# Kernel tuning notes

Hardware: AMD Instinct MI355X
Metric: run time of the kernel (lower is better)

The kernel has to match this reference:

```python
import jax, jax.numpy as jnp
import numpy as np

NP_, NA_ = 100_000, 50_000
E_ = 200_000
IN, HID, OUT = 128, 128, 128
HEADS = 4
D = HID // HEADS
# (src_node_type, dst_node_type) for edge types: cites, writes, written_by
EDGE_SPECS = [(0, 0), (1, 0), (0, 1)]
N_TYPES = 2
N_LAYERS = 2


def _rand_edges(key, e, n_src, n_dst):
    k1, k2 = jax.random.split(key)
    return jnp.stack([jax.random.randint(k1, (e,), 0, n_src),
                      jax.random.randint(k2, (e,), 0, n_dst)]).astype(jnp.int64)


def setup_inputs() -> dict:
    key = jax.random.key(0)
    ks = jax.random.split(key, 24)
    s = 0.05
    inp = {
        "x_paper": jax.random.normal(ks[0], (NP_, IN), jnp.float32),
        "x_author": jax.random.normal(ks[1], (NA_, IN), jnp.float32),
        "e_cites": _rand_edges(ks[2], E_, NP_, NP_),
        "e_writes": _rand_edges(ks[3], E_, NA_, NP_),
        "e_written": _rand_edges(ks[4], E_, NP_, NA_),
        # per-node-type input projection
        "lin_W": jax.random.normal(ks[5], (N_TYPES, IN, HID), jnp.float32) * s,
        "lin_b": jnp.zeros((N_TYPES, HID), jnp.float32),
        # per-layer, per-node-type K/Q/V projections
        "k_W": jax.random.normal(ks[6], (N_LAYERS, N_TYPES, HID, HID), jnp.float32) * s,
        "k_b": jnp.zeros((N_LAYERS, N_TYPES, HID), jnp.float32),
        "q_W": jax.random.normal(ks[7], (N_LAYERS, N_TYPES, HID, HID), jnp.float32) * s,
        "q_b": jnp.zeros((N_LAYERS, N_TYPES, HID), jnp.float32),
        "v_W": jax.random.normal(ks[8], (N_LAYERS, N_TYPES, HID, HID), jnp.float32) * s,
        "v_b": jnp.zeros((N_LAYERS, N_TYPES, HID), jnp.float32),
        # per-layer, per-node-type output projection a_lin
        "a_W": jax.random.normal(ks[9], (N_LAYERS, N_TYPES, HID, OUT), jnp.float32) * s,
        "a_b": jnp.zeros((N_LAYERS, N_TYPES, OUT), jnp.float32),
        # per-layer, per-node-type skip gate logit
        "skip": jnp.ones((N_LAYERS, N_TYPES), jnp.float32),
        # per-layer, per-edge-type relation matrices and priors
        "a_rel": jax.random.normal(ks[10], (N_LAYERS, 3, HEADS, D, D), jnp.float32) * s,
        "m_rel": jax.random.normal(ks[11], (N_LAYERS, 3, HEADS, D, D), jnp.float32) * s,
        "p_rel": jnp.ones((N_LAYERS, 3, HEADS), jnp.float32),
    }
    return inp


def _seg_softmax(logits, idx, n):
    m = jax.ops.segment_max(logits, idx, num_segments=n)  # [n,H]
    e = jnp.exp(logits - m[idx])
    s = jax.ops.segment_sum(e, idx, num_segments=n)
    return e / s[idx]


def _hgt_conv(xs, edges, kW, kb, qW, qb, vW, vb, aW, ab, skip, a_rel, m_rel, p_rel):
    ks = [(x @ kW[t] + kb[t]).reshape(-1, HEADS, D) for t, x in enumerate(xs)]
    qs = [(x @ qW[t] + qb[t]).reshape(-1, HEADS, D) for t, x in enumerate(xs)]
    vs = [(x @ vW[t] + vb[t]).reshape(-1, HEADS, D) for t, x in enumerate(xs)]
    acc = [jnp.zeros((x.shape[0], HEADS, D), x.dtype) for x in xs]
    scale = 1.0 / np.sqrt(D).astype(np.float32)
    for et, (s_t, d_t) in enumerate(EDGE_SPECS):
        src, dst = edges[et][0], edges[et][1]
        # relation-specific transform on the (smaller) node set, then gather
        kt = jnp.einsum('nhd,hde->nhe', ks[s_t], a_rel[et])
        vt = jnp.einsum('nhd,hde->nhe', vs[s_t], m_rel[et])
        n_dst = xs[d_t].shape[0]
        logits = (qs[d_t][dst] * kt[src]).sum(-1) * p_rel[et] * scale  # [E,H]
        att = _seg_softmax(logits, dst, n_dst)  # edge softmax per dst node (per edge type)
        msg = vt[src] * att[:, :, None]  # [E,H,D]
        acc[d_t] = acc[d_t] + jax.ops.segment_sum(msg, dst, num_segments=n_dst)
    outs = []
    for t, x in enumerate(xs):
        o = jax.nn.gelu(acc[t].reshape(x.shape[0], HID), approximate=False) @ aW[t] + ab[t]
        g = jax.nn.sigmoid(skip[t])  # out dim == in dim -> skip gate active
        outs.append(g * o + (1.0 - g) * x)
    return outs


def reference(x_paper, x_author, e_cites, e_writes, e_written,
              lin_W, lin_b, k_W, k_b, q_W, q_b, v_W, v_b,
              a_W, a_b, skip, a_rel, m_rel, p_rel):
    edges = [e_cites, e_writes, e_written]
    xs = [x_paper @ lin_W[0] + lin_b[0], x_author @ lin_W[1] + lin_b[1]]
    for L in range(N_LAYERS):
        xs = _hgt_conv(xs, edges, k_W[L], k_b[L], q_W[L], q_b[L], v_W[L], v_b[L],
                       a_W[L], a_b[L], skip[L], a_rel[L], m_rel[L], p_rel[L])
    return jnp.concatenate(xs, axis=0)  # [NP_+NA_, OUT]
```

## Files before the change

### kernel.cpp

```cpp
#include <hip/hip_runtime.h>
#include <math.h>

#define NPn 100000
#define NAn 50000
#define NTn 150000
#define En  200000
#define SCAN_N 250000

typedef short s16x8 __attribute__((ext_vector_type(8)));
typedef float f32x4 __attribute__((ext_vector_type(4)));

__device__ __forceinline__ unsigned short f2bfbits(float f) {
  unsigned u = __builtin_bit_cast(unsigned, f);
  return (unsigned short)((u + 0x7fffu + ((u >> 16) & 1u)) >> 16);
}
__device__ __forceinline__ float bf2f(unsigned short b) {
  return __builtin_bit_cast(float, (unsigned)b << 16);
}
__device__ __forceinline__ float gelu_f(float v) {
  return 0.5f * v * (1.f + erff(v * 0.70710678118654752f));
}

__device__ __forceinline__ void ldcol(const unsigned short* __restrict__ W, int lane, int ct, s16x8* b) {
  #pragma unroll
  for (int ks = 0; ks < 4; ++ks)
    b[ks] = *reinterpret_cast<const s16x8*>(W + ((size_t)(ks * 8 + ct) * 64 + lane) * 8);
}
__device__ __forceinline__ void mfma4(const s16x8* af, const s16x8* b, f32x4& acc) {
  #pragma unroll
  for (int ks = 0; ks < 4; ++ks)
    acc = __builtin_amdgcn_mfma_f32_16x16x32_bf16(af[ks], b[ks], acc, 0, 0, 0);
}

__global__ __launch_bounds__(256) void hist3_k(const int* __restrict__ e0, const int* __restrict__ e1,
                                               const int* __restrict__ e2, int* __restrict__ deg) {
  int i = blockIdx.x * 256 + threadIdx.x;
  int et = blockIdx.y;
  if (i >= En) return;
  const int* d = et == 0 ? e0 : (et == 1 ? e1 : e2);
  int etoff = et == 0 ? 0 : (et == 1 ? 100000 : 200000);
  atomicAdd(&deg[etoff + d[En + i]], 1);
}

__global__ __launch_bounds__(256) void scan1_k(const int* __restrict__ deg, int* __restrict__ bsum) {
  int t = threadIdx.x, lane = t & 63, wv = t >> 6;
  int base = blockIdx.x * 1024 + t * 4;
  int a0 = 0, a1 = 0, a2 = 0, a3 = 0;
  if (base + 3 < SCAN_N) {
    int4 v = *reinterpret_cast<const int4*>(deg + base);
    a0 = v.x; a1 = v.y; a2 = v.z; a3 = v.w;
  } else {
    if (base + 0 < SCAN_N) a0 = deg[base + 0];
    if (base + 1 < SCAN_N) a1 = deg[base + 1];
    if (base + 2 < SCAN_N) a2 = deg[base + 2];
    if (base + 3 < SCAN_N) a3 = deg[base + 3];
  }
  int s = a0 + a1 + a2 + a3;
  #pragma unroll
  for (int d = 1; d < 64; d <<= 1) s += __shfl_xor(s, d);
  __shared__ int wt[4];
  if (lane == 0) wt[wv] = s;
  __syncthreads();
  if (t == 0) bsum[blockIdx.x] = wt[0] + wt[1] + wt[2] + wt[3];
}

__global__ __launch_bounds__(256) void scan2_k(int* __restrict__ bsum, int nb) {
  int t = threadIdx.x, lane = t & 63, wv = t >> 6;
  int v = (t < nb) ? bsum[t] : 0;
  int x = v;
  #pragma unroll
  for (int d = 1; d < 64; d <<= 1) {
    int y = __shfl_up(x, d);
    if (lane >= d) x += y;
  }
  __shared__ int wt[4];
  if (lane == 63) wt[wv] = x;
  __syncthreads();
  int off = 0;
  for (int w = 0; w < wv; ++w) off += wt[w];
  if (t < nb) bsum[t] = x + off - v;
}

__global__ __launch_bounds__(256) void scan3_k(const int* __restrict__ deg, const int* __restrict__ bpre,
                                               int* __restrict__ S) {
  int t = threadIdx.x, lane = t & 63, wv = t >> 6;
  int base = blockIdx.x * 1024 + t * 4;
  int a[4] = {0, 0, 0, 0};
  if (base + 3 < SCAN_N) {
    int4 v = *reinterpret_cast<const int4*>(deg + base);
    a[0] = v.x; a[1] = v.y; a[2] = v.z; a[3] = v.w;
  } else {
    #pragma unroll
    for (int j = 0; j < 4; ++j) if (base + j < SCAN_N) a[j] = deg[base + j];
  }
  int s = a[0] + a[1] + a[2] + a[3];
  int x = s;
  #pragma unroll
  for (int d = 1; d < 64; d <<= 1) {
    int y = __shfl_up(x, d);
    if (lane >= d) x += y;
  }
  __shared__ int wt[4];
  if (lane == 63) wt[wv] = x;
  __syncthreads();
  int off = bpre[blockIdx.x];
  for (int w = 0; w < wv; ++w) off += wt[w];
  int ex = off + x - s;
  #pragma unroll
  for (int j = 0; j < 4; ++j) {
    int idx = base + j;
    if (idx < SCAN_N) {
      S[idx] = ex;
      ex += a[j];
      if (idx == SCAN_N - 1) S[SCAN_N] = ex;
    }
  }
}

__global__ __launch_bounds__(256) void fill3_k(const int* __restrict__ e0, const int* __restrict__ e1,
                                               const int* __restrict__ e2, int* cur, int* __restrict__ col) {
  int i = blockIdx.x * 256 + threadIdx.x;
  int et = blockIdx.y;
  if (i >= En) return;
  const int* ep = et == 0 ? e0 : (et == 1 ? e1 : e2);
  int etoff = et == 0 ? 0 : (et == 1 ? 100000 : 200000);
  int p = atomicAdd(&cur[etoff + ep[En + i]], 1);
  col[p] = ep[i];
}

__global__ __launch_bounds__(256) void fuse_k(const float* __restrict__ kW, const float* __restrict__ kb,
                                              const float* __restrict__ vW, const float* __restrict__ vb,
                                              const float* __restrict__ a_rel, const float* __restrict__ m_rel,
                                              float* __restrict__ Wf, float* __restrict__ bfv) {
  int b = blockIdx.x;
  int L = b / 6, et = (b % 6) / 2, which = b & 1;
  int s_t = (et == 1) ? 1 : 0;
  const float* W = which ? vW : kW;
  const float* bb = which ? vb : kb;
  const float* R = which ? m_rel : a_rel;
  const float* Wsrc = W + (size_t)(L * 2 + s_t) * 128 * 128;
  const float* bsrc = bb + (size_t)(L * 2 + s_t) * 128;
  const float* Rsrc = R + (size_t)(L * 3 + et) * 4 * 32 * 32;
  float* Wdst = Wf + (size_t)b * 128 * 128;
  float* bdst = bfv + (size_t)b * 128;
  for (int idx = threadIdx.x; idx < 128 * 128; idx += 256) {
    int i = idx >> 7, c = idx & 127;
    int h = c >> 5, cc = c & 31;
    const float* r = Rsrc + (size_t)h * 32 * 32 + cc;
    const float* w = Wsrc + (size_t)i * 128 + h * 32;
    float s = 0.f;
    #pragma unroll 8
    for (int d = 0; d < 32; ++d) s += w[d] * r[d * 32];
    Wdst[idx] = s;
  }
  for (int c = threadIdx.x; c < 128; c += 256) {
    int h = c >> 5, cc = c & 31;
    float s = 0.f;
    for (int d = 0; d < 32; ++d) s += bsrc[h * 32 + d] * Rsrc[((size_t)h * 32 + d) * 32 + cc];
    bdst[c] = s;
  }
}

__global__ __launch_bounds__(256) void pack_k(const float* __restrict__ linW, const float* __restrict__ qW,
                                              const float* __restrict__ aW, const float* __restrict__ Wf,
                                              unsigned short* __restrict__ Wp) {
  int m = blockIdx.x;
  const float* src;
  if (m < 2) src = linW + (size_t)m * 16384;
  else if (m < 6) src = qW + (size_t)(m - 2) * 16384;
  else if (m < 18) src = Wf + (size_t)(m - 6) * 16384;
  else src = aW + (size_t)(m - 18) * 16384;
  int lane = threadIdx.x & 63, wv = threadIdx.x >> 6;
  unsigned short* dst = Wp + (size_t)m * 16384;
  for (int ct = 0; ct < 8; ++ct) {
    s16x8 t;
    #pragma unroll
    for (int i = 0; i < 8; ++i) {
      int k = wv * 32 + (lane >> 4) * 8 + i;
      int n = ct * 16 + (lane & 15);
      t[i] = (short)f2bfbits(src[k * 128 + n]);
    }
    *reinterpret_cast<s16x8*>(dst + ((size_t)(wv * 8 + ct) * 64 + lane) * 8) = t;
  }
}

struct IJob { const float* X; const unsigned short* W; const float* bias; unsigned short* Y; int N; };

__global__ __launch_bounds__(256, 4) void iproj_k(IJob ja, IJob jb) {
  IJob j = blockIdx.y ? jb : ja;
  int ntj = (j.N + 63) >> 6;
  int tile = blockIdx.x;
  if (tile >= ntj) return;
  int lane = threadIdx.x & 63, wv = threadIdx.x >> 6;
  int t = threadIdx.x;
  int rl = j.N - tile * 64; if (rl > 64) rl = 64;

  __shared__ float xin[64 * 132];
  {
    const uint4* src = reinterpret_cast<const uint4*>(j.X + (size_t)tile * 64 * 128);
    uint4* dst = reinterpret_cast<uint4*>(xin);
    for (int c = t; c < 2048; c += 256) {
      int row = c >> 5;
      if (row < rl) dst[row * 33 + (c & 31)] = src[c];
    }
  }
  __syncthreads();

  int lr = wv * 16 + (lane & 15);
  s16x8 af[4];
  #pragma unroll
  for (int ks = 0; ks < 4; ++ks) {
    const float* p = xin + lr * 132 + (lane >> 4) * 8 + ks * 32;
    s16x8 tt;
    #pragma unroll
    for (int i = 0; i < 8; ++i) tt[i] = (short)f2bfbits(p[i]);
    af[ks] = tt;
  }

  float bias_[8];
  #pragma unroll
  for (int ct = 0; ct < 8; ++ct) bias_[ct] = j.bias[ct * 16 + (lane & 15)];

  f32x4 acc[8];
  #pragma unroll
  for (int ct = 0; ct < 8; ++ct) acc[ct] = (f32x4){0.f, 0.f, 0.f, 0.f};

  s16x8 bA[4], bB[4];
  ldcol(j.W, lane, 0, bA);
  ldcol(j.W, lane, 1, bB);
  mfma4(af, bA, acc[0]); ldcol(j.W, lane, 2, bA);
  mfma4(af, bB, acc[1]); ldcol(j.W, lane, 3, bB);
  mfma4(af, bA, acc[2]); ldcol(j.W, lane, 4, bA);
  mfma4(af, bB, acc[3]); ldcol(j.W, lane, 5, bB);
  mfma4(af, bA, acc[4]); ldcol(j.W, lane, 6, bA);
  mfma4(af, bB, acc[5]); ldcol(j.W, lane, 7, bB);
  mfma4(af, bA, acc[6]);
  mfma4(af, bB, acc[7]);

  __syncthreads();
  unsigned short* ot = reinterpret_cast<unsigned short*>(xin);
  int c0 = lane & 15, r00 = wv * 16 + (lane >> 4) * 4;
  #pragma unroll
  for (int ct = 0; ct < 8; ++ct)
    #pragma unroll
    for (int i = 0; i < 4; ++i)
      ot[(r00 + i) * 132 + ct * 16 + c0] = f2bfbits(acc[ct][i] + bias_[ct]);
  __syncthreads();
  {
    unsigned int* dstU = reinterpret_cast<unsigned int*>(j.Y + (size_t)tile * 64 * 128);
    for (int c = t; c < 4096; c += 256) {
      int row = c >> 6, col2 = c & 63;
      if (row < rl) dstU[row * 64 + col2] = *reinterpret_cast<const unsigned int*>(ot + row * 132 + col2 * 2);
    }
  }
}

struct QKVJob {
  const unsigned short* X; int N; int nm; int pad;
  const unsigned short* W[5];
  const float* bias[5];
  unsigned short* Y[5];
};

__global__ __launch_bounds__(256, 3) void qkv_k(QKVJob ja, QKVJob jb) {
  QKVJob j = blockIdx.y ? jb : ja;
  int ntj = (j.N + 127) >> 7;
  int tile = blockIdx.x;
  if (tile >= ntj) return;
  int lane = threadIdx.x & 63, wv = threadIdx.x >> 6;
  int t = threadIdx.x;
  int rbase = tile * 128;
  int rl = j.N - rbase; if (rl > 128) rl = 128;

  s16x8 af0[4], af1[4];
  {
    int ar = rbase + wv * 16 + (lane & 15); if (ar >= j.N) ar = j.N - 1;
    const unsigned short* xp = j.X + (size_t)ar * 128 + (lane >> 4) * 8;
    #pragma unroll
    for (int ks = 0; ks < 4; ++ks) af0[ks] = *reinterpret_cast<const s16x8*>(xp + ks * 32);
  }
  {
    int ar = rbase + 64 + wv * 16 + (lane & 15); if (ar >= j.N) ar = j.N - 1;
    const unsigned short* xp = j.X + (size_t)ar * 128 + (lane >> 4) * 8;
    #pragma unroll
    for (int ks = 0; ks < 4; ++ks) af1[ks] = *reinterpret_cast<const s16x8*>(xp + ks * 32);
  }

  __shared__ unsigned short ot[2][64 * 132];
  int c0 = lane & 15, r00 = wv * 16 + (lane >> 4) * 4;

  s16x8 bA[4], bB[4];
  ldcol(j.W[0], lane, 0, bA);

  for (int m = 0; m < j.nm; ++m) {
    const unsigned short* Wm = j.W[m];
    float bias_[8];
    #pragma unroll
    for (int ct = 0; ct < 8; ++ct) bias_[ct] = j.bias[m][ct * 16 + (lane & 15)];

    f32x4 acc0[8], acc1[8];
    #pragma unroll
    for (int ct = 0; ct < 8; ++ct) { acc0[ct] = (f32x4){0.f, 0.f, 0.f, 0.f}; acc1[ct] = (f32x4){0.f, 0.f, 0.f, 0.f}; }

    ldcol(Wm, lane, 1, bB);
    mfma4(af0, bA, acc0[0]); mfma4(af1, bA, acc1[0]); ldcol(Wm, lane, 2, bA);
    mfma4(af0, bB, acc0[1]); mfma4(af1, bB, acc1[1]); ldcol(Wm, lane, 3, bB);
    mfma4(af0, bA, acc0[2]); mfma4(af1, bA, acc1[2]); ldcol(Wm, lane, 4, bA);
    mfma4(af0, bB, acc0[3]); mfma4(af1, bB, acc1[3]); ldcol(Wm, lane, 5, bB);
    mfma4(af0, bA, acc0[4]); mfma4(af1, bA, acc1[4]); ldcol(Wm, lane, 6, bA);
    mfma4(af0, bB, acc0[5]); mfma4(af1, bB, acc1[5]); ldcol(Wm, lane, 7, bB);
    mfma4(af0, bA, acc0[6]); mfma4(af1, bA, acc1[6]);
    if (m + 1 < j.nm) ldcol(j.W[m + 1], lane, 0, bA);
    mfma4(af0, bB, acc0[7]); mfma4(af1, bB, acc1[7]);

    if (m) __syncthreads();
    #pragma unroll
    for (int ct = 0; ct < 8; ++ct)
      #pragma unroll
      for (int i = 0; i < 4; ++i) {
        ot[0][(r00 + i) * 132 + ct * 16 + c0] = f2bfbits(acc0[ct][i] + bias_[ct]);
        ot[1][(r00 + i) * 132 + ct * 16 + c0] = f2bfbits(acc1[ct][i] + bias_[ct]);
      }
    __syncthreads();
    unsigned int* dstU = reinterpret_cast<unsigned int*>(j.Y[m] + (size_t)rbase * 128);
    for (int c = t; c < 8192; c += 256) {
      int row = c >> 6, col2 = c & 63;
      if (row < rl)
        dstU[row * 64 + col2] =
            *reinterpret_cast<const unsigned int*>(&ot[row >> 6][(row & 63) * 132 + col2 * 2]);
    }
  }
}

struct OJob {
  const unsigned short* G;
  const unsigned short* W;
  const float* bias;
  const unsigned short* skip;
  const float* skp;
  unsigned short* Yb;
  float* Yf;
  int N;
};

template <int FINAL>
__global__ __launch_bounds__(256, 4) void oproj_k(OJob ja, OJob jb) {
  OJob j = blockIdx.y ? jb : ja;
  int ntj = (j.N + 63) >> 6;
  int tile = blockIdx.x;
  if (tile >= ntj) return;
  int lane = threadIdx.x & 63, wv = threadIdx.x >> 6;
  int t = threadIdx.x;
  int rl = j.N - tile * 64; if (rl > 64) rl = 64;

  __shared__ unsigned short sk[64 * 132];
  {
    const unsigned int* srcU = reinterpret_cast<const unsigned int*>(j.skip + (size_t)tile * 64 * 128);
    for (int c = t; c < 4096; c += 256) {
      int row = c >> 6, col2 = c & 63;
      if (row < rl) *reinterpret_cast<unsigned int*>(sk + row * 132 + col2 * 2) = srcU[row * 64 + col2];
    }
  }

  int arow = tile * 64 + wv * 16 + (lane & 15);
  if (arow >= j.N) arow = j.N - 1;
  const unsigned short* xp = j.G + (size_t)arow * 128 + (lane >> 4) * 8;
  s16x8 af[4];
  #pragma unroll
  for (int ks = 0; ks < 4; ++ks) af[ks] = *reinterpret_cast<const s16x8*>(xp + ks * 32);

  float bias_[8];
  #pragma unroll
  for (int ct = 0; ct < 8; ++ct) bias_[ct] = j.bias[ct * 16 + (lane & 15)];
  float g = 1.f / (1.f + __expf(-*j.skp));

  f32x4 acc[8];
  #pragma unroll
  for (int ct = 0; ct < 8; ++ct) acc[ct] = (f32x4){0.f, 0.f, 0.f, 0.f};

  s16x8 bA[4], bB[4];
  ldcol(j.W, lane, 0, bA);
  ldcol(j.W, lane, 1, bB);
  mfma4(af, bA, acc[0]); ldcol(j.W, lane, 2, bA);
  mfma4(af, bB, acc[1]); ldcol(j.W, lane, 3, bB);
  mfma4(af, bA, acc[2]); ldcol(j.W, lane, 4, bA);
  mfma4(af, bB, acc[3]); ldcol(j.W, lane, 5, bB);
  mfma4(af, bA, acc[4]); ldcol(j.W, lane, 6, bA);
  mfma4(af, bB, acc[5]); ldcol(j.W, lane, 7, bB);
  mfma4(af, bA, acc[6]);
  mfma4(af, bB, acc[7]);

  __syncthreads();
  int c0 = lane & 15, r00 = wv * 16 + (lane >> 4) * 4;
  if (FINAL) {
    float* yf = j.Yf + (size_t)tile * 64 * 128;
    #pragma unroll
    for (int ct = 0; ct < 8; ++ct)
      #pragma unroll
      for (int i = 0; i < 4; ++i) {
        int r = r00 + i;
        if (r < rl) {
          float y = g * (acc[ct][i] + bias_[ct]) + (1.f - g) * bf2f(sk[r * 132 + ct * 16 + c0]);
          yf[r * 128 + ct * 16 + c0] = y;
        }
      }
  } else {
    #pragma unroll
    for (int ct = 0; ct < 8; ++ct)
      #pragma unroll
      for (int i = 0; i < 4; ++i) {
        int idx = (r00 + i) * 132 + ct * 16 + c0;
        float y = g * (acc[ct][i] + bias_[ct]) + (1.f - g) * bf2f(sk[idx]);
        sk[idx] = f2bfbits(y);
      }
    __syncthreads();
    unsigned int* dstU = reinterpret_cast<unsigned int*>(j.Yb + (size_t)tile * 64 * 128);
    for (int c = t; c < 4096; c += 256) {
      int row = c >> 6, col2 = c & 63;
      if (row < rl) dstU[row * 64 + col2] = *reinterpret_cast<const unsigned int*>(sk + row * 132 + col2 * 2);
    }
  }
}

__global__ __launch_bounds__(256) void attn_k(const int* __restrict__ S, const int* __restrict__ col,
                                              const unsigned short* __restrict__ kt,
                                              const unsigned short* __restrict__ vt,
                                              const unsigned short* __restrict__ qb,
                                              unsigned short* __restrict__ gbuf,
                                              const float* __restrict__ prelL) {
  int node = (blockIdx.x * 256 + threadIdx.x) >> 6;
  if (node >= NTn) return;
  int lane = threadIdx.x & 63;
  int h = lane >> 4;
  bool isP = node < NPn;
  int ln = isP ? node : node - NPn;

  ushort2 qv = *reinterpret_cast<const ushort2*>(qb + (size_t)node * 128 + lane * 2);
  float q0 = bf2f(qv.x), q1 = bf2f(qv.y);

  float facc0 = 0.f, facc1 = 0.f;
  int np = isP ? 2 : 1;
  for (int p = 0; p < np; ++p) {
    int soff   = isP ? (p ? 100000 : 0) : 200000;
    int ktbase = isP ? (p ? 100000 : 0) : 150000;
    const float* prp = prelL + (isP ? p * 4 : 8);
    float pr = prp[h] * 0.17677669529663687f;
    int rs = S[soff + ln], re = S[soff + ln + 1];
    if (rs >= re) continue;
    const unsigned short* ktb = kt + (size_t)ktbase * 128;
    const unsigned short* vtb = vt + (size_t)ktbase * 128;
    float m = -3.0e38f, den = 0.f, n0 = 0.f, n1 = 0.f;
    for (int base = rs; base < re; base += 4) {
      int n = re - base; if (n > 4) n = 4;
      int sidx[4];
      #pragma unroll
      for (int jj = 0; jj < 4; ++jj) sidx[jj] = col[base + (jj < n ? jj : 0)];
      ushort2 kvv[4], vvv[4];
      #pragma unroll
      for (int jj = 0; jj < 4; ++jj) {
        kvv[jj] = *reinterpret_cast<const ushort2*>(ktb + (size_t)sidx[jj] * 128 + lane * 2);
        vvv[jj] = *reinterpret_cast<const ushort2*>(vtb + (size_t)sidx[jj] * 128 + lane * 2);
      }
      #pragma unroll
      for (int jj = 0; jj < 4; ++jj) {
        if (jj < n) {
          float pdot = q0 * bf2f(kvv[jj].x) + q1 * bf2f(kvv[jj].y);
          pdot += __shfl_xor(pdot, 1); pdot += __shfl_xor(pdot, 2);
          pdot += __shfl_xor(pdot, 4); pdot += __shfl_xor(pdot, 8);
          float pm = pdot * pr;
          float nm = fmaxf(m, pm);
          float sc = __expf(m - nm);
          float w = __expf(pm - nm);
          den = den * sc + w;
          n0 = n0 * sc + w * bf2f(vvv[jj].x);
          n1 = n1 * sc + w * bf2f(vvv[jj].y);
          m = nm;
        }
      }
    }
    float inv = 1.f / den;
    facc0 += n0 * inv;
    facc1 += n1 * inv;
  }
  ushort2 o;
  o.x = f2bfbits(gelu_f(facc0));
  o.y = f2bfbits(gelu_f(facc1));
  *reinterpret_cast<ushort2*>(gbuf + (size_t)node * 128 + lane * 2) = o;
}

extern "C" void kernel_launch(void* const* d_in, const int* in_sizes, int n_in,
                              void* d_out, int out_size, void* d_ws, size_t ws_size,
                              hipStream_t stream) {
  const float* x_paper  = (const float*)d_in[0];
  const float* x_author = (const float*)d_in[1];
  const int* e[3] = {(const int*)d_in[2], (const int*)d_in[3], (const int*)d_in[4]};
  const float* linW = (const float*)d_in[5];
  const float* linb = (const float*)d_in[6];
  const float* kW = (const float*)d_in[7];
  const float* kb = (const float*)d_in[8];
  const float* qW = (const float*)d_in[9];
  const float* qbv = (const float*)d_in[10];
  const float* vW = (const float*)d_in[11];
  const float* vb = (const float*)d_in[12];
  const float* aW = (const float*)d_in[13];
  const float* ab = (const float*)d_in[14];
  const float* skipv = (const float*)d_in[15];
  const float* a_rel = (const float*)d_in[16];
  const float* m_rel = (const float*)d_in[17];
  const float* prel  = (const float*)d_in[18];

  char* ws = (char*)d_ws;
  size_t off = 0;
  auto alloc = [&](size_t b) { char* p = ws + off; off = (off + b + 255) & ~(size_t)255; return p; };
  unsigned short* qbuf = (unsigned short*)alloc((size_t)NTn * 128 * 2);
  unsigned short* ktA  = (unsigned short*)alloc((size_t)SCAN_N * 128 * 2);
  unsigned short* vtA  = (unsigned short*)alloc((size_t)SCAN_N * 128 * 2);
  unsigned short* gbuf = (unsigned short*)alloc((size_t)NTn * 128 * 2);
  unsigned short* xb   = (unsigned short*)alloc((size_t)NTn * 128 * 2);
  int* deg   = (int*)alloc((size_t)SCAN_N * 4);
  int* cur   = (int*)alloc((size_t)SCAN_N * 4);
  int* S     = (int*)alloc((size_t)(SCAN_N + 1) * 4);
  int* bsum  = (int*)alloc(256 * 4);
  int* col   = (int*)alloc((size_t)3 * En * 4);
  float* Wf  = (float*)alloc((size_t)12 * 16384 * 4);
  float* bfv = (float*)alloc((size_t)12 * 128 * 4);
  unsigned short* Wp = (unsigned short*)alloc((size_t)22 * 16384 * 2);

  hipMemsetAsync(deg, 0, (size_t)SCAN_N * 4, stream);
  hist3_k<<<dim3(782, 3), 256, 0, stream>>>(e[0], e[1], e[2], deg);
  scan1_k<<<245, 256, 0, stream>>>(deg, bsum);
  scan2_k<<<1, 256, 0, stream>>>(bsum, 245);
  scan3_k<<<245, 256, 0, stream>>>(deg, bsum, S);
  hipMemcpyAsync(cur, S, (size_t)SCAN_N * 4, hipMemcpyDeviceToDevice, stream);
  fill3_k<<<dim3(782, 3), 256, 0, stream>>>(e[0], e[1], e[2], cur, col);

  fuse_k<<<12, 256, 0, stream>>>(kW, kb, vW, vb, a_rel, m_rel, Wf, bfv);
  pack_k<<<22, 256, 0, stream>>>(linW, qW, aW, Wf, Wp);

  {
    IJob jp  = {x_paper,  Wp + 0 * 16384, linb,        xb,                       NPn};
    IJob jat = {x_author, Wp + 1 * 16384, linb + 128,  xb + (size_t)NPn * 128,   NAn};
    iproj_k<<<dim3(1563, 2), 256, 0, stream>>>(jp, jat);
  }

  const int ktbases[3] = {0, 100000, 150000};

  for (int L = 0; L < 2; ++L) {
    {
      QKVJob jp{}, jat{};
      jp.X = xb; jp.N = NPn; jp.nm = 5;
      jp.W[0] = Wp + (size_t)(2 + L * 2) * 16384;      jp.bias[0] = qbv + (L * 2) * 128;             jp.Y[0] = qbuf;
      jp.W[1] = Wp + (size_t)(6 + L * 6 + 0) * 16384;  jp.bias[1] = bfv + (size_t)(L * 6 + 0) * 128; jp.Y[1] = ktA + (size_t)ktbases[0] * 128;
      jp.W[2] = Wp + (size_t)(6 + L * 6 + 1) * 16384;  jp.bias[2] = bfv + (size_t)(L * 6 + 1) * 128; jp.Y[2] = vtA + (size_t)ktbases[0] * 128;
      jp.W[3] = Wp + (size_t)(6 + L * 6 + 4) * 16384;  jp.bias[3] = bfv + (size_t)(L * 6 + 4) * 128; jp.Y[3] = ktA + (size_t)ktbases[2] * 128;
      jp.W[4] = Wp + (size_t)(6 + L * 6 + 5) * 16384;  jp.bias[4] = bfv + (size_t)(L * 6 + 5) * 128; jp.Y[4] = vtA + (size_t)ktbases[2] * 128;
      jat.X = xb + (size_t)NPn * 128; jat.N = NAn; jat.nm = 3;
      jat.W[0] = Wp + (size_t)(3 + L * 2) * 16384;     jat.bias[0] = qbv + (L * 2 + 1) * 128;         jat.Y[0] = qbuf + (size_t)NPn * 128;
      jat.W[1] = Wp + (size_t)(6 + L * 6 + 2) * 16384; jat.bias[1] = bfv + (size_t)(L * 6 + 2) * 128; jat.Y[1] = ktA + (size_t)ktbases[1] * 128;
      jat.W[2] = Wp + (size_t)(6 + L * 6 + 3) * 16384; jat.bias[2] = bfv + (size_t)(L * 6 + 3) * 128; jat.Y[2] = vtA + (size_t)ktbases[1] * 128;
      qkv_k<<<dim3(782, 2), 256, 0, stream>>>(jp, jat);
    }
    attn_k<<<37500, 256, 0, stream>>>(S, col, ktA, vtA, qbuf, gbuf, prel + (size_t)L * 12);
    {
      OJob jp  = {gbuf, Wp + (size_t)(18 + L * 2) * 16384, ab + (L * 2) * 128,
                  xb, skipv + L * 2, xb, (float*)d_out, NPn};
      OJob jat = {gbuf + (size_t)NPn * 128, Wp + (size_t)(19 + L * 2) * 16384, ab + (L * 2 + 1) * 128,
                  xb + (size_t)NPn * 128, skipv + L * 2 + 1, xb + (size_t)NPn * 128,
                  (float*)d_out + (size_t)NPn * 128, NAn};
      if (L == 0) oproj_k<0><<<dim3(1563, 2), 256, 0, stream>>>(jp, jat);
      else        oproj_k<1><<<dim3(1563, 2), 256, 0, stream>>>(jp, jat);
    }
  }
}
```

Measured before the change: 673.2 us.

## Split attention wavefront into two halves processing interleaved edges, merge softmax states

The per-node attention kernel now splits each 64-lane wavefront into two 32-lane halves. Each half handles every other edge of the node's neighbour list, with each lane covering 4 channels through 8-byte loads instead of 2 channels. The two partial online-softmax states (max, denominator, numerators) are merged with cross-half shuffles before normalisation and GELU, and only the first half writes the result. This is meant to shorten the serial per-edge dependency chain, cut the shuffle reduction by one step, and widen the gather loads. The cost is extra merge exps and shuffles, and half the lanes sit idle for the final write.

```diff
diff --git a/kernel.cpp b/kernel.cpp
--- a/kernel.cpp
+++ b/kernel.cpp
@@ -431,61 +431,78 @@
   int node = (blockIdx.x * 256 + threadIdx.x) >> 6;
   if (node >= NTn) return;
   int lane = threadIdx.x & 63;
-  int h = lane >> 4;
+  int half = lane >> 5, hl = lane & 31;
+  int h = hl >> 3;
+  int coff = h * 32 + (hl & 7) * 4;
   bool isP = node < NPn;
   int ln = isP ? node : node - NPn;
 
-  ushort2 qv = *reinterpret_cast<const ushort2*>(qb + (size_t)node * 128 + lane * 2);
-  float q0 = bf2f(qv.x), q1 = bf2f(qv.y);
-
-  float facc0 = 0.f, facc1 = 0.f;
+  float q0, q1, q2, q3;
+  {
+    ushort4 qv = *reinterpret_cast<const ushort4*>(qb + (size_t)node * 128 + coff);
+    q0 = bf2f(qv.x); q1 = bf2f(qv.y); q2 = bf2f(qv.z); q3 = bf2f(qv.w);
+  }
+
+  float facc0 = 0.f, facc1 = 0.f, facc2 = 0.f, facc3 = 0.f;
   int np = isP ? 2 : 1;
-  for (int p = 0; p < np; ++p) {
-    int soff   = isP ? (p ? 100000 : 0) : 200000;
-    int ktbase = isP ? (p ? 100000 : 0) : 150000;
-    const float* prp = prelL + (isP ? p * 4 : 8);
-    float pr = prp[h] * 0.17677669529663687f;
+  for (int pp = 0; pp < np; ++pp) {
+    int soff   = isP ? (pp ? 100000 : 0) : 200000;
+    int ktbase = isP ? (pp ? 100000 : 0) : 150000;
+    float pr = prelL[(isP ? pp * 4 : 8) + h] * 0.17677669529663687f;
     int rs = S[soff + ln], re = S[soff + ln + 1];
     if (rs >= re) continue;
-    const unsigned short* ktb = kt + (size_t)ktbase * 128;
-    const unsigned short* vtb = vt + (size_t)ktbase * 128;
-    float m = -3.0e38f, den = 0.f, n0 = 0.f, n1 = 0.f;
-    for (int base = rs; base < re; base += 4) {
-      int n = re - base; if (n > 4) n = 4;
-      int sidx[4];
-      #pragma unroll
-      for (int jj = 0; jj < 4; ++jj) sidx[jj] = col[base + (jj < n ? jj : 0)];
-      ushort2 kvv[4], vvv[4];
-      #pragma unroll
-      for (int jj = 0; jj < 4; ++jj) {
-        kvv[jj] = *reinterpret_cast<const ushort2*>(ktb + (size_t)sidx[jj] * 128 + lane * 2);
-        vvv[jj] = *reinterpret_cast<const ushort2*>(vtb + (size_t)sidx[jj] * 128 + lane * 2);
+    const unsigned short* ktb = kt + (size_t)ktbase * 128 + coff;
+    const unsigned short* vtb = vt + (size_t)ktbase * 128 + coff;
+    float m = -3.0e38f, den = 0.f, n0 = 0.f, n1 = 0.f, n2 = 0.f, n3 = 0.f;
+    for (int base = rs + half; base < re; base += 4) {
+      int i1 = base + 2;
+      bool has1 = i1 < re;
+      int s0 = col[base];
+      int s1 = has1 ? col[i1] : s0;
+      ushort4 k0 = *reinterpret_cast<const ushort4*>(ktb + (size_t)s0 * 128);
+      ushort4 v0 = *reinterpret_cast<const ushort4*>(vtb + (size_t)s0 * 128);
+      ushort4 k1 = *reinterpret_cast<const ushort4*>(ktb + (size_t)s1 * 128);
+      ushort4 v1 = *reinterpret_cast<const ushort4*>(vtb + (size_t)s1 * 128);
+      float pd = q0 * bf2f(k0.x) + q1 * bf2f(k0.y) + q2 * bf2f(k0.z) + q3 * bf2f(k0.w);
+      pd += __shfl_xor(pd, 1); pd += __shfl_xor(pd, 2); pd += __shfl_xor(pd, 4);
+      float pm = pd * pr;
+      float nm = fmaxf(m, pm);
+      float sc = __expf(m - nm), w = __expf(pm - nm);
+      den = den * sc + w;
+      n0 = n0 * sc + w * bf2f(v0.x); n1 = n1 * sc + w * bf2f(v0.y);
+      n2 = n2 * sc + w * bf2f(v0.z); n3 = n3 * sc + w * bf2f(v0.w);
+      m = nm;
+      if (has1) {
+        pd = q0 * bf2f(k1.x) + q1 * bf2f(k1.y) + q2 * bf2f(k1.z) + q3 * bf2f(k1.w);
+        pd += __shfl_xor(pd, 1); pd += __shfl_xor(pd, 2); pd += __shfl_xor(pd, 4);
+        pm = pd * pr;
+        nm = fmaxf(m, pm);
+        sc = __expf(m - nm); w = __expf(pm - nm);
+        den = den * sc + w;
+        n0 = n0 * sc + w * bf2f(v1.x); n1 = n1 * sc + w * bf2f(v1.y);
+        n2 = n2 * sc + w * bf2f(v1.z); n3 = n3 * sc + w * bf2f(v1.w);
+        m = nm;
       }
-      #pragma unroll
-      for (int jj = 0; jj < 4; ++jj) {
-        if (jj < n) {
-          float pdot = q0 * bf2f(kvv[jj].x) + q1 * bf2f(kvv[jj].y);
-          pdot += __shfl_xor(pdot, 1); pdot += __shfl_xor(pdot, 2);
-          pdot += __shfl_xor(pdot, 4); pdot += __shfl_xor(pdot, 8);
-          float pm = pdot * pr;
-          float nm = fmaxf(m, pm);
-          float sc = __expf(m - nm);
-          float w = __expf(pm - nm);
-          den = den * sc + w;
-          n0 = n0 * sc + w * bf2f(vvv[jj].x);
-          n1 = n1 * sc + w * bf2f(vvv[jj].y);
-          m = nm;
-        }
-      }
-    }
-    float inv = 1.f / den;
-    facc0 += n0 * inv;
-    facc1 += n1 * inv;
-  }
-  ushort2 o;
-  o.x = f2bfbits(gelu_f(facc0));
-  o.y = f2bfbits(gelu_f(facc1));
-  *reinterpret_cast<ushort2*>(gbuf + (size_t)node * 128 + lane * 2) = o;
+    }
+    float mo   = __shfl_xor(m, 32);
+    float deno = __shfl_xor(den, 32);
+    float no0 = __shfl_xor(n0, 32), no1 = __shfl_xor(n1, 32);
+    float no2 = __shfl_xor(n2, 32), no3 = __shfl_xor(n3, 32);
+    float ms = fmaxf(m, mo);
+    float scs = __expf(m - ms), sco = __expf(mo - ms);
+    float dent = den * scs + deno * sco;
+    float inv = 1.f / dent;
+    facc0 += (n0 * scs + no0 * sco) * inv;
+    facc1 += (n1 * scs + no1 * sco) * inv;
+    facc2 += (n2 * scs + no2 * sco) * inv;
+    facc3 += (n3 * scs + no3 * sco) * inv;
+  }
+  if (half == 0) {
+    ushort4 o;
+    o.x = f2bfbits(gelu_f(facc0)); o.y = f2bfbits(gelu_f(facc1));
+    o.z = f2bfbits(gelu_f(facc2)); o.w = f2bfbits(gelu_f(facc3));
+    *reinterpret_cast<ushort4*>(gbuf + (size_t)node * 128 + coff) = o;
+  }
 }
 
 extern "C" void kernel_launch(void* const* d_in, const int* in_sizes, int n_in,
```

New measurement: 656.6 us. 1.03x faster.
